# Performance work log

Hardware: AMD Instinct MI355X
Metric: run time of the kernel (lower is better)

Reference implementation:

```python
import jax, jax.numpy as jnp
import numpy as np

KS, STRIDE, PAD = 3, 1, 1
IN_C, OUT_C = 64, 128
EPS = 1e-12
P_SCALE, Q_SCALE = 10.0, 100.0


def unfold2d(x, ks, stride, pad):
    # x: [n, c, h, w] -> [n, c, oh, ow, ks*ks], patch index l = i*ks + j
    x = jnp.pad(x, ((0, 0), (0, 0), (pad, pad), (pad, pad)))
    n, c, H, W = x.shape
    oh = (H - ks) // stride + 1
    ow = (W - ks) // stride + 1
    patches = [x[:, :, i:i + stride * oh:stride, j:j + stride * ow:stride]
               for i in range(ks) for j in range(ks)]
    return jnp.stack(patches, axis=-1)


def setup_inputs() -> dict:
    key = jax.random.key(0)
    k1, k2 = jax.random.split(key)
    x = jax.random.normal(k1, (32, IN_C, 56, 56), dtype=jnp.float32)
    # xavier_uniform over (out, in, ks, ks): bound = sqrt(6/(fan_in+fan_out))
    fan_in = IN_C * KS * KS
    fan_out = OUT_C * KS * KS
    bound = float(np.sqrt(6.0 / (fan_in + fan_out)))
    w = jax.random.uniform(k2, (OUT_C, IN_C, KS * KS), dtype=jnp.float32,
                           minval=-bound, maxval=bound)
    p = jnp.full((OUT_C,), (2.0 ** 0.5) * P_SCALE, dtype=jnp.float32)
    q = jnp.full((1,), 10.0, dtype=jnp.float32)
    return {"x": x, "w": w, "p": p, "q": q}


def reference(x, w, p, q):
    patches = unfold2d(x, KS, STRIDE, PAD)            # [n, c, h, w, l]
    q2 = jnp.square(q / Q_SCALE)                      # [1]
    # patch norms over (c, l)
    x_ss = jnp.sum(jnp.square(patches), axis=(1, 4), keepdims=True)
    x_norm = jnp.sqrt(x_ss + EPS) + q2                # [n,1,h,w,1]
    # weight norms over (c, l)
    w_ss = jnp.sum(jnp.square(w), axis=(1, 2), keepdims=True)
    w_norm = jnp.sqrt(w_ss + EPS) + q2                # [v,1,1]
    out = jnp.einsum('nchwl,vcl->nvhw', patches / x_norm, w / w_norm)
    sign = jnp.sign(out)
    mag = jnp.abs(out) + EPS
    exp = jnp.square(p / P_SCALE).reshape(1, -1, 1, 1)
    return sign * jnp.power(mag, exp)
```

## Files before the change

kernel.cpp:

```cpp
#include <hip/hip_runtime.h>
#include <math.h>
#include <stdint.h>

#define IN_C 64
#define OUT_C 128
#define H 56
#define W 56
#define NB 32
#define HW (H*W)
#define KK 576
#define EPS 1e-12f
#define PH 58
#define PW 66

#define XT_BYTES 44544
#define WT_BYTES 16384
#define CONV_LDS (XT_BYTES + 2 * WT_BYTES)

typedef _Float16 half8 __attribute__((ext_vector_type(8)));
typedef float f32x4 __attribute__((ext_vector_type(4)));
typedef unsigned int u32;
typedef const u32 __attribute__((address_space(1)))* gp_t;
typedef u32 __attribute__((address_space(3)))* sp_t;

__global__ __launch_bounds__(256) void k_xpose(const float* __restrict__ x,
                                               _Float16* __restrict__ xcl,
                                               float* __restrict__ s) {
    __shared__ float lds[64][59];
    int n = blockIdx.y, pr = blockIdx.x;
    int tid = threadIdx.x;
    int h = pr - 1;
    bool rowz = (h < 0 || h >= H);
    {
        int w = tid & 63, c4 = tid >> 6;
        if (!rowz && w < 56) {
#pragma unroll
            for (int cg = 0; cg < 16; ++cg) {
                int c = cg * 4 + c4;
                lds[c][w] = x[((size_t)(n * IN_C + c)) * HW + h * W + w];
            }
        }
    }
    __syncthreads();
    int c = tid & 63, pg = tid >> 6;
    _Float16* dst = xcl + ((size_t)n * PH + pr) * PW * IN_C;
#pragma unroll
    for (int pcg = 0; pcg < 15; ++pcg) {
        int pc = pcg * 4 + pg;
        if (pc >= 58) break;
        int w = pc - 1;
        bool valid = (!rowz && (unsigned)w < W);
        float val = valid ? lds[c][w] : 0.f;
        dst[(size_t)pc * IN_C + (c ^ ((pc & 7) << 3))] = (_Float16)val;
        float sq = val * val;
#pragma unroll
        for (int off = 32; off > 0; off >>= 1) sq += __shfl_xor(sq, off);
        if (valid && c == 0) s[(size_t)n * HW + h * W + w] = sq;
    }
}

__global__ __launch_bounds__(256) void k_xnorm(const float* __restrict__ s,
                                               const float* __restrict__ q,
                                               float* __restrict__ inv_xn) {
    int t = blockIdx.x * 256 + threadIdx.x;
    if (t >= NB * HW / 4) return;
    int n = t / (HW / 4);
    int rem = t - n * (HW / 4);
    int p0 = rem * 4;
    int h = p0 / W, w0 = p0 - h * W;
    float q2 = q[0] * 0.01f;
    q2 = q2 * q2;
    const float* sp = s + (size_t)n * HW;
    float a0 = 0.f, a1 = 0.f, a2 = 0.f, a3 = 0.f;
#pragma unroll
    for (int dy = -1; dy <= 1; ++dy) {
        int y = h + dy;
        if ((unsigned)y >= H) continue;
        const float* row = sp + y * W;
        float4 m = *(const float4*)(row + w0);
        float lft = (w0 > 0) ? row[w0 - 1] : 0.f;
        float rgt = (w0 + 4 < W) ? row[w0 + 4] : 0.f;
        a0 += lft + m.x + m.y;
        a1 += m.x + m.y + m.z;
        a2 += m.y + m.z + m.w;
        a3 += m.z + m.w + rgt;
    }
    float4 res;
    res.x = 1.f / (sqrtf(a0 + EPS) + q2);
    res.y = 1.f / (sqrtf(a1 + EPS) + q2);
    res.z = 1.f / (sqrtf(a2 + EPS) + q2);
    res.w = 1.f / (sqrtf(a3 + EPS) + q2);
    *(float4*)(inv_xn + (size_t)n * HW + p0) = res;
}

__global__ __launch_bounds__(64) void k_wprep(const float* __restrict__ w,
                                              const float* __restrict__ p,
                                              const float* __restrict__ q,
                                              _Float16* __restrict__ wt,
                                              float* __restrict__ e) {
    int v = blockIdx.x;
    int lane = threadIdx.x;
    const float* wv = w + v * KK;
    float acc = 0.f;
#pragma unroll
    for (int j = 0; j < 9; ++j) {
        float t = wv[lane * 9 + j];
        acc += t * t;
    }
#pragma unroll
    for (int off = 32; off > 0; off >>= 1) acc += __shfl_xor(acc, off);
    float q2 = q[0] * 0.01f;
    q2 = q2 * q2;
    float inv = 1.f / (sqrtf(acc + EPS) + q2);
    int cs = lane ^ ((v & 7) << 3);
#pragma unroll
    for (int l = 0; l < 9; ++l) {
        wt[((size_t)l * OUT_C + v) * IN_C + cs] = (_Float16)(wv[lane * 9 + l] * inv);
    }
    if (lane == 0) e[v] = p[v] * p[v] * 0.01f;
}

__global__ __launch_bounds__(512, 4) void k_conv_mfma(
    const _Float16* __restrict__ xcl,
    const _Float16* __restrict__ wt,
    const float* __restrict__ inv_xn,
    const float* __restrict__ e,
    float* __restrict__ out)
{
    extern __shared__ __align__(16) char smem[];
    char* xls = smem;
    char* wls = smem + XT_BYTES;

    int tid = threadIdx.x;
    int wv = tid >> 6;
    int lane = tid & 63;
    int l15 = lane & 15;
    int kg = lane >> 4;

    int flat = blockIdx.y * 14 + blockIdx.x;
    int sw = (flat & 7) * 56 + (flat >> 3);
    int n = sw / 14;
    int rc = sw - n * 14;
    int r0 = rc * 4;
    int row_rel = wv >> 1;
    int vh = wv & 1;
    int wave_chunk = wv * 64;

    {
        const char* xsrc = (const char*)(xcl + ((size_t)n * PH + r0) * PW * IN_C);
#pragma unroll
        for (int i = 0; i < 6; ++i) {
            int j = i * 512 + tid;
            if (j < 2784) {
                int row = j / 464;
                int off = j - row * 464;
                __builtin_amdgcn_global_load_lds(
                    (gp_t)(xsrc + row * (PW * IN_C * 2) + off * 16),
                    (sp_t)(xls + (i * 512 + wave_chunk) * 16), 16, 0, 0);
            }
        }
        const char* wsrc = (const char*)wt;
#pragma unroll
        for (int i = 0; i < 2; ++i)
            __builtin_amdgcn_global_load_lds(
                (gp_t)(wsrc + (i * 512 + tid) * 16),
                (sp_t)(wls + (i * 512 + wave_chunk) * 16), 16, 0, 0);
    }

    f32x4 acc[4][4];
#pragma unroll
    for (int mt = 0; mt < 4; ++mt)
#pragma unroll
        for (int vt = 0; vt < 4; ++vt) acc[mt][vt] = (f32x4){0.f, 0.f, 0.f, 0.f};

#pragma unroll
    for (int l = 0; l < 9; ++l) {
        if (l < 8) {
            const char* wsrc = (const char*)wt + (size_t)(l + 1) * WT_BYTES;
            char* wdst = wls + ((l + 1) & 1) * WT_BYTES;
            __builtin_amdgcn_global_load_lds(
                (gp_t)(wsrc + tid * 16),
                (sp_t)(wdst + wave_chunk * 16), 16, 0, 0);
            __builtin_amdgcn_global_load_lds(
                (gp_t)(wsrc + (512 + tid) * 16),
                (sp_t)(wdst + (512 + wave_chunk) * 16), 16, 0, 0);
        }
        if (l < 8) asm volatile("s_waitcnt vmcnt(2)" ::: "memory");
        else       asm volatile("s_waitcnt vmcnt(0)" ::: "memory");
        __builtin_amdgcn_s_barrier();

        int di = l / 3, dj = l % 3;
        int pc0 = l15 + dj;
        const char* xb = xls + ((row_rel + di) * 58 + pc0) * 128;
        int xkey = (pc0 & 7) << 4;
        const char* wb = wls + (l & 1) * WT_BYTES + (vh * 64 + l15) * 128;
        int wkey = (l15 & 7) << 4;

#pragma unroll
        for (int k = 0; k < 2; ++k) {
            int ko = k * 64 + kg * 16;
            half8 a[4];
#pragma unroll
            for (int mt = 0; mt < 4; ++mt)
                a[mt] = *(const half8*)(xb + mt * 2048 + (ko ^ xkey));
            half8 b[4];
#pragma unroll
            for (int vt = 0; vt < 4; ++vt)
                b[vt] = *(const half8*)(wb + vt * 2048 + (ko ^ wkey));
            __builtin_amdgcn_s_setprio(1);
#pragma unroll
            for (int vt = 0; vt < 4; ++vt)
#pragma unroll
                for (int mt = 0; mt < 4; ++mt)
                    acc[mt][vt] = __builtin_amdgcn_mfma_f32_16x16x32_f16(
                        a[mt], b[vt], acc[mt][vt], 0, 0, 0);
            __builtin_amdgcn_s_setprio(0);
        }
        __builtin_amdgcn_s_barrier();
    }

    int r = r0 + row_rel;
    const float* ixrow = inv_xn + (size_t)n * HW + r * W;
#pragma unroll
    for (int mt = 0; mt < 4; ++mt) {
        int col0 = mt * 16 + kg * 4;
        if (col0 >= W) continue;
        float4 ixn = *(const float4*)(ixrow + col0);
        const float* ixp = &ixn.x;
#pragma unroll
        for (int vt = 0; vt < 4; ++vt) {
            int v = vh * 64 + vt * 16 + l15;
            float ev = e[v];
            float4 res;
            float* rp = &res.x;
            if (fabsf(ev - 2.0f) < 1e-4f) {
#pragma unroll
                for (int j = 0; j < 4; ++j) {
                    float z = acc[mt][vt][j] * ixp[j];
                    float mag = fabsf(z) + EPS;
                    rp[j] = copysignf(mag * mag, z);
                }
            } else {
#pragma unroll
                for (int j = 0; j < 4; ++j) {
                    float z = acc[mt][vt][j] * ixp[j];
                    float mag = fabsf(z) + EPS;
                    float pw = exp2f(ev * log2f(mag));
                    rp[j] = copysignf(pw, z);
                }
            }
            *(float4*)(out + ((size_t)n * OUT_C + v) * HW + r * W + col0) = res;
        }
    }
}

extern "C" void kernel_launch(void* const* d_in, const int* in_sizes, int n_in,
                              void* d_out, int out_size, void* d_ws, size_t ws_size,
                              hipStream_t stream) {
    const float* x = (const float*)d_in[0];
    const float* w = (const float*)d_in[1];
    const float* p = (const float*)d_in[2];
    const float* q = (const float*)d_in[3];
    float* out = (float*)d_out;

    char* ws = (char*)d_ws;
    float*    s      = (float*)ws;
    float*    inv_xn = (float*)(ws + 401408);
    float*    e      = (float*)(ws + 802816);
    _Float16* wt     = (_Float16*)(ws + 803328);
    _Float16* xcl    = (_Float16*)(ws + 950784);

    hipFuncSetAttribute((const void*)k_conv_mfma,
                        hipFuncAttributeMaxDynamicSharedMemorySize, CONV_LDS);

    k_xpose<<<dim3(PH, NB), dim3(256), 0, stream>>>(x, xcl, s);
    k_xnorm<<<dim3(NB * HW / 4 / 256), dim3(256), 0, stream>>>(s, q, inv_xn);
    k_wprep<<<dim3(OUT_C), dim3(64), 0, stream>>>(w, p, q, wt, e);
    k_conv_mfma<<<dim3(14, NB), dim3(512), CONV_LDS, stream>>>(
        xcl, wt, inv_xn, e, out);
}
```

Before: 52.11 us.

## Triple-buffer weight tiles and register double-buffer LDS fragments in conv kernel

The weight tile for each of the 9 taps now streams through three LDS slots instead of two, with DMA issued three taps ahead. The A and B fragments for the next taps are prefetched into two register buffers with inline ds_read_b128 and explicit lgkmcnt waits, so the MFMA loop runs from registers already loaded. The goal is to hide LDS read latency and global-to-LDS weight latency behind the MFMAs. In exchange, LDS per block grows, which likely allows only one block per CU instead of two. Launch bounds are lowered to 2 to give more registers, and occupancy may drop as a result.

```diff
diff --git a/kernel.cpp b/kernel.cpp
--- a/kernel.cpp
+++ b/kernel.cpp
@@ -14,8 +14,8 @@
 #define PW 66
 
 #define XT_BYTES 44544
-#define WT_BYTES 16384
-#define CONV_LDS (XT_BYTES + 2 * WT_BYTES)
+#define WSLOT 16384
+#define CONV_LDS (XT_BYTES + 3 * WSLOT)
 
 typedef _Float16 half8 __attribute__((ext_vector_type(8)));
 typedef float f32x4 __attribute__((ext_vector_type(4)));
@@ -120,7 +120,7 @@
     if (lane == 0) e[v] = p[v] * p[v] * 0.01f;
 }
 
-__global__ __launch_bounds__(512, 4) void k_conv_mfma(
+__global__ __launch_bounds__(512, 2) void k_conv_mfma(
     const _Float16* __restrict__ xcl,
     const _Float16* __restrict__ wt,
     const float* __restrict__ inv_xn,
@@ -146,6 +146,15 @@
     int vh = wv & 1;
     int wave_chunk = wv * 64;
 
+#define WDMA(t) do {                                                          \
+        const char* wsrc_ = (const char*)wt + (size_t)(t) * WSLOT;            \
+        char* wdst_ = wls + ((t) % 3) * WSLOT;                                \
+        __builtin_amdgcn_global_load_lds((gp_t)(wsrc_ + tid * 16),            \
+            (sp_t)(wdst_ + wave_chunk * 16), 16, 0, 0);                       \
+        __builtin_amdgcn_global_load_lds((gp_t)(wsrc_ + (512 + tid) * 16),    \
+            (sp_t)(wdst_ + (512 + wave_chunk) * 16), 16, 0, 0);               \
+    } while (0)
+
     {
         const char* xsrc = (const char*)(xcl + ((size_t)n * PH + r0) * PW * IN_C);
 #pragma unroll
@@ -159,13 +168,41 @@
                     (sp_t)(xls + (i * 512 + wave_chunk) * 16), 16, 0, 0);
             }
         }
-        const char* wsrc = (const char*)wt;
-#pragma unroll
-        for (int i = 0; i < 2; ++i)
-            __builtin_amdgcn_global_load_lds(
-                (gp_t)(wsrc + (i * 512 + tid) * 16),
-                (sp_t)(wls + (i * 512 + wave_chunk) * 16), 16, 0, 0);
-    }
+        WDMA(0); WDMA(1); WDMA(2);
+    }
+    asm volatile("s_waitcnt vmcnt(2)" ::: "memory");
+    __builtin_amdgcn_s_barrier();
+
+    u32 xb32 = (u32)(uintptr_t)(sp_t)xls;
+    u32 wb32 = (u32)(uintptr_t)(sp_t)wls;
+
+    half8 fa[2][2][4];
+    half8 fb[2][2][4];
+
+#define ISSUE_READS(t) do {                                                   \
+        const int di_ = (t) / 3, dj_ = (t) % 3;                               \
+        int pc0_ = l15 + dj_;                                                 \
+        u32 xa_ = xb32 + (u32)(((row_rel + di_) * 58 + pc0_) * 128);          \
+        int xk_ = (pc0_ & 7) << 4;                                            \
+        u32 wa_ = wb32 + (u32)(((t) % 3) * WSLOT + (vh * 64 + l15) * 128);    \
+        int wk_ = (l15 & 7) << 4;                                             \
+        _Pragma("unroll") for (int k_ = 0; k_ < 2; ++k_) {                    \
+            int ko_ = k_ * 64 + kg * 16;                                      \
+            _Pragma("unroll") for (int mt_ = 0; mt_ < 4; ++mt_)               \
+                asm volatile("ds_read_b128 %0, %1"                            \
+                    : "=v"(fa[(t) & 1][k_][mt_])                              \
+                    : "v"(xa_ + (u32)(mt_ * 2048) + (u32)(ko_ ^ xk_)));       \
+            _Pragma("unroll") for (int vt_ = 0; vt_ < 4; ++vt_)               \
+                asm volatile("ds_read_b128 %0, %1"                            \
+                    : "=v"(fb[(t) & 1][k_][vt_])                              \
+                    : "v"(wa_ + (u32)(vt_ * 2048) + (u32)(ko_ ^ wk_)));       \
+        }                                                                     \
+    } while (0)
+
+    ISSUE_READS(0);
+    ISSUE_READS(1);
+    asm volatile("s_waitcnt lgkmcnt(15)" ::: "memory");
+    __builtin_amdgcn_sched_barrier(0);
 
     f32x4 acc[4][4];
 #pragma unroll
@@ -175,49 +212,32 @@
 
 #pragma unroll
     for (int l = 0; l < 9; ++l) {
-        if (l < 8) {
-            const char* wsrc = (const char*)wt + (size_t)(l + 1) * WT_BYTES;
-            char* wdst = wls + ((l + 1) & 1) * WT_BYTES;
-            __builtin_amdgcn_global_load_lds(
-                (gp_t)(wsrc + tid * 16),
-                (sp_t)(wdst + wave_chunk * 16), 16, 0, 0);
-            __builtin_amdgcn_global_load_lds(
-                (gp_t)(wsrc + (512 + tid) * 16),
-                (sp_t)(wdst + (512 + wave_chunk) * 16), 16, 0, 0);
-        }
-        if (l < 8) asm volatile("s_waitcnt vmcnt(2)" ::: "memory");
-        else       asm volatile("s_waitcnt vmcnt(0)" ::: "memory");
-        __builtin_amdgcn_s_barrier();
-
-        int di = l / 3, dj = l % 3;
-        int pc0 = l15 + dj;
-        const char* xb = xls + ((row_rel + di) * 58 + pc0) * 128;
-        int xkey = (pc0 & 7) << 4;
-        const char* wb = wls + (l & 1) * WT_BYTES + (vh * 64 + l15) * 128;
-        int wkey = (l15 & 7) << 4;
-
-#pragma unroll
-        for (int k = 0; k < 2; ++k) {
-            int ko = k * 64 + kg * 16;
-            half8 a[4];
-#pragma unroll
-            for (int mt = 0; mt < 4; ++mt)
-                a[mt] = *(const half8*)(xb + mt * 2048 + (ko ^ xkey));
-            half8 b[4];
-#pragma unroll
-            for (int vt = 0; vt < 4; ++vt)
-                b[vt] = *(const half8*)(wb + vt * 2048 + (ko ^ wkey));
-            __builtin_amdgcn_s_setprio(1);
+        __builtin_amdgcn_s_setprio(1);
+#pragma unroll
+        for (int k = 0; k < 2; ++k)
 #pragma unroll
             for (int vt = 0; vt < 4; ++vt)
 #pragma unroll
                 for (int mt = 0; mt < 4; ++mt)
                     acc[mt][vt] = __builtin_amdgcn_mfma_f32_16x16x32_f16(
-                        a[mt], b[vt], acc[mt][vt], 0, 0, 0);
-            __builtin_amdgcn_s_setprio(0);
-        }
+                        fa[l & 1][k][mt], fb[l & 1][k][vt], acc[mt][vt], 0, 0, 0);
+        __builtin_amdgcn_s_setprio(0);
+
         __builtin_amdgcn_s_barrier();
-    }
+        if (l + 3 <= 8) WDMA(l + 3);
+        if (l < 8) {
+            asm volatile("s_waitcnt lgkmcnt(0)" ::: "memory");
+            __builtin_amdgcn_sched_barrier(0);
+        }
+        if (l + 2 <= 8) {
+            if (l + 3 <= 8) asm volatile("s_waitcnt vmcnt(2)" ::: "memory");
+            else            asm volatile("s_waitcnt vmcnt(0)" ::: "memory");
+            __builtin_amdgcn_s_barrier();
+            ISSUE_READS(l + 2);
+        }
+    }
+#undef ISSUE_READS
+#undef WDMA
 
     int r = r0 + row_rel;
     const float* ixrow = inv_xn + (size_t)n * HW + r * W;
@@ -270,7 +290,7 @@
     _Float16* wt     = (_Float16*)(ws + 803328);
     _Float16* xcl    = (_Float16*)(ws + 950784);
 
-    hipFuncSetAttribute((const void*)k_conv_mfma,
+    (void)hipFuncSetAttribute((const void*)k_conv_mfma,
                         hipFuncAttributeMaxDynamicSharedMemorySize, CONV_LDS);
 
     k_xpose<<<dim3(PH, NB), dim3(256), 0, stream>>>(x, xcl, s);
```

New measurement: 55.98 us. 7.4% more time.
